# Kernel tuning notes

Hardware: AMD Instinct MI355X
Metric: run time of the kernel (lower is better)

## Reference

```python
import jax, jax.numpy as jnp
import numpy as np

N_HEAD, D_MODEL, D_K, D_V = 16, 1024, 64, 64
BIAS_WEIGHT = 1.0
NEG = -10000.0


def setup_inputs() -> dict:
    key = jax.random.key(0)
    ks = jax.random.split(key, 9)
    B, L = 2, 2048
    q = jax.random.normal(ks[0], (B, L, D_MODEL), dtype=jnp.float32)
    k = jax.random.normal(ks[1], (B, L, D_MODEL), dtype=jnp.float32)
    v = jax.random.normal(ks[2], (B, L, D_MODEL), dtype=jnp.float32)
    mask = jax.random.randint(ks[3], (B, L, L), 0, 2, dtype=jnp.int32)
    bias = jax.random.normal(ks[4], (B, L, L), dtype=jnp.float32)
    s = 1.0 / np.sqrt(D_MODEL)
    w_qs = jax.random.uniform(ks[5], (D_MODEL, N_HEAD * D_K), jnp.float32, -s, s)
    w_ks = jax.random.uniform(ks[6], (D_MODEL, N_HEAD * D_K), jnp.float32, -s, s)
    w_vs = jax.random.uniform(ks[7], (D_MODEL, N_HEAD * D_V), jnp.float32, -s, s)
    w_fc = jax.random.uniform(ks[8], (N_HEAD * D_V, D_MODEL), jnp.float32, -s, s)
    return {"q": q, "k": k, "v": v, "mask": mask, "bias": bias,
            "w_qs": w_qs, "w_ks": w_ks, "w_vs": w_vs, "w_fc": w_fc}


def reference(q, k, v, mask, bias, w_qs, w_ks, w_vs, w_fc):
    B, Lq, _ = q.shape
    # project and split heads: [B, H, L, d]
    qh = (q @ w_qs).reshape(B, Lq, N_HEAD, D_K).transpose(0, 2, 1, 3)
    kh = (k @ w_ks).reshape(B, k.shape[1], N_HEAD, D_K).transpose(0, 2, 1, 3)
    vh = (v @ w_vs).reshape(B, v.shape[1], N_HEAD, D_V).transpose(0, 2, 1, 3)
    temperature = D_K ** 0.5
    attn = jnp.einsum('bhqd,bhkd->bhqk', qh / temperature, kh)
    attn = attn + bias[:, None, :, :] * BIAS_WEIGHT
    attn = jnp.where(mask[:, None, :, :] == 0, NEG, attn)
    attn = jax.nn.softmax(attn, axis=-1)
    out = jnp.einsum('bhqk,bhkd->bhqd', attn, vh)
    out = out.transpose(0, 2, 1, 3).reshape(B, Lq, N_HEAD * D_V)
    return out @ w_fc
```

## Files before the change

kernel.cpp:

```cpp
#include <hip/hip_runtime.h>
#include <cstddef>

#define DEV static __device__ __forceinline__

typedef float f32x4 __attribute__((ext_vector_type(4)));
typedef __bf16 bf16x8 __attribute__((ext_vector_type(8)));
typedef __bf16 bf16x4v __attribute__((ext_vector_type(4)));
typedef unsigned short u16x8 __attribute__((ext_vector_type(8)));
typedef unsigned short u16x4 __attribute__((ext_vector_type(4)));
typedef unsigned u32x2 __attribute__((ext_vector_type(2)));
typedef unsigned u32x4 __attribute__((ext_vector_type(4)));
typedef _Float16 f16;
typedef _Float16 f16x4 __attribute__((ext_vector_type(4)));

constexpr int BB = 2, LL = 2048, DM = 1024, NH = 16, DK = 64;
constexpr float LOG2E = 1.44269504f;

DEV unsigned short f2bf(float f) {
  unsigned u = __builtin_bit_cast(unsigned, f);
  u += 0x7fffu + ((u >> 16) & 1u);
  return (unsigned short)(u >> 16);
}
DEV u16x4 cvt4(f32x4 v) {
  bf16x4v b = __builtin_convertvector(v, bf16x4v);
  return __builtin_bit_cast(u16x4, b);
}
DEV bf16x8 asbf(u16x8 v) { return __builtin_bit_cast(bf16x8, v); }
DEV f32x4 mfma16(u16x8 a, u16x8 b, f32x4 c) {
  return __builtin_amdgcn_mfma_f32_16x16x32_bf16(asbf(a), asbf(b), c, 0, 0, 0);
}
#if __has_builtin(__builtin_amdgcn_exp2f)
DEV float fexp2(float x) { return __builtin_amdgcn_exp2f(x); }
#else
DEV float fexp2(float x) { return exp2f(x); }
#endif
DEV void swap32(unsigned& a, unsigned& b) {
#if __has_builtin(__builtin_amdgcn_permlane32_swap)
  u32x2 r = __builtin_amdgcn_permlane32_swap(a, b, false, false);
  a = r[0]; b = r[1];
#else
  asm("v_permlane32_swap_b32 %0, %1" : "+v"(a), "+v"(b));
#endif
}
DEV void swap16(unsigned& a, unsigned& b) {
#if __has_builtin(__builtin_amdgcn_permlane16_swap)
  u32x2 r = __builtin_amdgcn_permlane16_swap(a, b, false, false);
  a = r[0]; b = r[1];
#else
  asm("v_permlane16_swap_b32 %0, %1" : "+v"(a), "+v"(b));
#endif
}
DEV void g2lds16(const void* g, void* l) {
  __builtin_amdgcn_global_load_lds(
      (const __attribute__((address_space(1))) unsigned int*)g,
      (__attribute__((address_space(3))) unsigned int*)l, 16, 0, 0);
}

__global__ __launch_bounds__(256) void prep_all(
    const float* __restrict__ w0, const float* __restrict__ w1,
    const float* __restrict__ w2, const float* __restrict__ w3,
    unsigned short* __restrict__ wT, const int* __restrict__ mask,
    const float* __restrict__ bias, f16* __restrict__ bmf,
    const float* __restrict__ s0, const float* __restrict__ s1,
    const float* __restrict__ s2, unsigned short* __restrict__ qkvb) {
  int f = blockIdx.x, t = threadIdx.x;
  if (f < 4096) {
    __shared__ float tile[32][33];
    int z = f >> 10, rem = f & 1023;
    int k0 = (rem >> 5) * 32, n0 = (rem & 31) * 32;
    const float* W = (z == 0) ? w0 : (z == 1) ? w1 : (z == 2) ? w2 : w3;
    unsigned short* out = wT + (size_t)z * DM * DM;
    int tx = t & 31, ty = t >> 5;
#pragma unroll
    for (int p = 0; p < 4; p++)
      tile[ty + 8 * p][tx] = W[(size_t)(k0 + ty + 8 * p) * DM + n0 + tx];
    __syncthreads();
#pragma unroll
    for (int p = 0; p < 4; p++)
      out[(size_t)(n0 + ty + 8 * p) * DM + k0 + tx] = f2bf(tile[tx][ty + 8 * p]);
  } else if (f < 12288) {
    int f2 = f - 4096;
    int w = t >> 6, lane = t & 63;
    int bq = f2 >> 5;
    int kt = (f2 & 31) * 4 + w;
    int b = bq >> 7, qt = bq & 127;
    int q = qt * 16 + (lane & 15);
    int k = kt * 16 + (lane >> 4) * 4;
    size_t src = ((size_t)b * LL + q) * LL + k;
    int4 mk = *(const int4*)(mask + src);
    float4 bs = *(const float4*)(bias + src);
    f16x4 o;
    o[0] = (f16)((mk.x == 0 ? -10000.f : bs.x) * LOG2E);
    o[1] = (f16)((mk.y == 0 ? -10000.f : bs.y) * LOG2E);
    o[2] = (f16)((mk.z == 0 ? -10000.f : bs.z) * LOG2E);
    o[3] = (f16)((mk.w == 0 ? -10000.f : bs.w) * LOG2E);
    *(f16x4*)(bmf + ((size_t)bq * 128 + kt) * 256 + lane * 4) = o;
  } else {
    int f3 = f - 12288;
    int z = f3 >> 11;
    const float* src = (z == 0) ? s0 : (z == 1) ? s1 : s2;
    size_t i = ((size_t)(f3 & 2047) * 256 + t) * 8;
    float4 a = *(const float4*)(src + i);
    float4 b = *(const float4*)(src + i + 4);
    u16x8 o;
    o[0] = f2bf(a.x); o[1] = f2bf(a.y); o[2] = f2bf(a.z); o[3] = f2bf(a.w);
    o[4] = f2bf(b.x); o[5] = f2bf(b.y); o[6] = f2bf(b.z); o[7] = f2bf(b.w);
    *(u16x8*)(qkvb + (size_t)z * (size_t)(BB * LL) * DM + i) = o;
  }
}

template <int KITERS>
DEV void gemm_core(const unsigned short* __restrict__ A,
                   const unsigned short* __restrict__ BT,
                   unsigned short* Al, unsigned short* Bl,
                   int m0, int n0, int k0beg, int t, f32x4 (&acc)[4][4]) {
  int lane = t & 63, c = lane & 15, qd = lane >> 4;
  int w = t >> 6, wm = w >> 1, wn = w & 1;
  int r0 = t >> 3;
  int gsw = (t & 7) ^ (r0 & 7);

#pragma unroll 1
  for (int kk = 0; kk < KITERS; ++kk) {
    int k0 = k0beg + kk * 64;
#pragma unroll
    for (int p = 0; p < 4; ++p) {
      g2lds16(&A[(size_t)(m0 + 32 * p + r0) * DM + k0 + 8 * gsw],
              &Al[p * 2048 + w * 512]);
      g2lds16(&BT[(size_t)(n0 + 32 * p + r0) * DM + k0 + 8 * gsw],
              &Bl[p * 2048 + w * 512]);
    }
    __syncthreads();
#pragma unroll
    for (int ks = 0; ks < 2; ++ks) {
      u16x8 af[4], bfr[4];
#pragma unroll
      for (int mt = 0; mt < 4; ++mt)
        af[mt] = *(const u16x8*)&Al[(64 * wm + 16 * mt + c) * 64 +
                                    (((4 * ks + qd) ^ (c & 7)) << 3)];
#pragma unroll
      for (int nt = 0; nt < 4; ++nt)
        bfr[nt] = *(const u16x8*)&Bl[(64 * wn + 16 * nt + c) * 64 +
                                     (((4 * ks + qd) ^ (c & 7)) << 3)];
#pragma unroll
      for (int mt = 0; mt < 4; ++mt)
#pragma unroll
        for (int nt = 0; nt < 4; ++nt)
          acc[mt][nt] = mfma16(af[mt], bfr[nt], acc[mt][nt]);
    }
    __syncthreads();
  }
}

__global__ __launch_bounds__(256, 3) void proj_gemm(
    const unsigned short* __restrict__ qkvb, const unsigned short* __restrict__ wT,
    unsigned short* __restrict__ qh, unsigned short* __restrict__ kh,
    unsigned short* __restrict__ vT) {
  __shared__ unsigned short Al[128 * 64];
  __shared__ unsigned short Bl[128 * 64];
  int o = blockIdx.x;
  int wg = (o & 7) * 96 + (o >> 3);
  int z = wg >> 8, rem = wg & 255;
  int m0 = (rem >> 3) * 128, n0 = (rem & 7) * 128;
  const unsigned short* A = qkvb + (size_t)z * BB * LL * DM;
  const unsigned short* BT = wT + (size_t)z * DM * DM;
  int t = threadIdx.x, lane = t & 63, c = lane & 15, qd = lane >> 4;
  int w = t >> 6, wm = w >> 1, wn = w & 1;
  f32x4 acc[4][4] = {};
  gemm_core<DM / 64>(A, BT, Al, Bl, m0, n0, 0, t, acc);

  if (z == 2) {
#pragma unroll
    for (int mt = 0; mt < 4; ++mt)
#pragma unroll
      for (int nt = 0; nt < 4; ++nt) {
        int n = n0 + 64 * wn + 16 * nt + c;
        int h = n >> 6, d = n & 63;
        int m = m0 + 64 * wm + 16 * mt + 4 * qd;
        int b = m >> 11, l = m & 2047;
        *(u16x4*)&vT[(((size_t)b * NH + h) * DK + d) * LL + l] = cvt4(acc[mt][nt]);
      }
  } else {
    unsigned short* Ch = z ? kh : qh;
    float scale = z ? 1.0f : 0.125f * LOG2E;
#pragma unroll
    for (int mt = 0; mt < 4; ++mt)
#pragma unroll
      for (int nt = 0; nt < 4; ++nt) {
        int n = n0 + 64 * wn + 16 * nt + c;
        int h = n >> 6, d = n & 63;
#pragma unroll
        for (int i = 0; i < 4; ++i) {
          int m = m0 + 64 * wm + 16 * mt + 4 * qd + i;
          int b = m >> 11, l = m & 2047;
          Ch[(((size_t)b * NH + h) * LL + l) * DK + d] = f2bf(acc[mt][nt][i] * scale);
        }
      }
  }
}

__global__ __launch_bounds__(256, 3) void fc_gemm(const unsigned short* __restrict__ A,
                                                  const unsigned short* __restrict__ BT,
                                                  float* __restrict__ C) {
  __shared__ unsigned short Al[128 * 64];
  __shared__ unsigned short Bl[128 * 64];
  int o = blockIdx.x;
  int wg = (o & 7) * 32 + (o >> 3);
  int m0 = (wg >> 3) * 128, n0 = (wg & 7) * 128;
  int t = threadIdx.x, lane = t & 63, c = lane & 15, qd = lane >> 4;
  int w = t >> 6, wm = w >> 1, wn = w & 1;
  f32x4 acc[4][4] = {};
  gemm_core<DM / 64>(A, BT, Al, Bl, m0, n0, 0, t, acc);
#pragma unroll
  for (int mt = 0; mt < 4; ++mt)
#pragma unroll
    for (int nt = 0; nt < 4; ++nt) {
      int n = n0 + 64 * wn + 16 * nt + c;
#pragma unroll
      for (int i = 0; i < 4; ++i) {
        int m = m0 + 64 * wm + 16 * mt + 4 * qd + i;
        C[(size_t)m * DM + n] = acc[mt][nt][i];
      }
    }
}

__global__ __launch_bounds__(256, 4) void attn_kern(
    const unsigned short* __restrict__ qh, const unsigned short* __restrict__ kh,
    const unsigned short* __restrict__ vT, const f16* __restrict__ bmf,
    unsigned short* __restrict__ O) {
  __shared__ unsigned short Kb[2][4096];
  __shared__ unsigned short Vb[3][4096];

  int t = threadIdx.x, w = t >> 6, lane = t & 63, c = lane & 15, qd = lane >> 4;
  int o = blockIdx.x;
  int wg = (o & 7) * 128 + (o >> 3);
  int x = wg & 31, h = (wg >> 5) & 15, b = wg >> 9;
  int q0 = x * 64;
  const unsigned short* Q = qh + (((size_t)b * NH + h) * LL + q0) * DK;
  const unsigned short* K = kh + ((size_t)b * NH + h) * LL * DK;
  const unsigned short* V = vT + ((size_t)b * NH + h) * DK * LL;
  const f16* BMF = bmf + (((size_t)b * 128 + x * 4 + w) * 128) * 256 + lane * 4;
  int rt = t >> 3, gg = t & 7;

  f16x4 bc[4], bn[4];
#pragma unroll
  for (int r = 0; r < 2; ++r) {
    int row = r * 32 + rt;
    int sc = ((gg ^ (row & 7)) << 3);
    g2lds16(&Q[(size_t)row * DK + sc], &Kb[1][r * 2048 + w * 512]);
    g2lds16(&K[(size_t)row * DK + sc], &Kb[0][r * 2048 + w * 512]);
    g2lds16(&V[(size_t)row * LL + sc], &Vb[0][r * 2048 + w * 512]);
  }
#pragma unroll
  for (int mt = 0; mt < 4; ++mt) bc[mt] = *(const f16x4*)&BMF[(size_t)mt * 256];
  __syncthreads();

  u16x8 qf[2];
#pragma unroll
  for (int ks = 0; ks < 2; ++ks)
    qf[ks] = *(const u16x8*)&Kb[1][(16 * w + c) * 64 +
                                   (((4 * ks + qd) ^ (c & 7)) << 3)];
  __syncthreads();

  {
#pragma unroll
    for (int r = 0; r < 2; ++r) {
      int row = r * 32 + rt;
      int sc = ((gg ^ (row & 7)) << 3);
      g2lds16(&K[(size_t)(64 + row) * DK + sc], &Kb[1][r * 2048 + w * 512]);
      g2lds16(&V[(size_t)row * LL + 64 + sc], &Vb[1][r * 2048 + w * 512]);
    }
#pragma unroll
    for (int mt = 0; mt < 4; ++mt)
      bn[mt] = *(const f16x4*)&BMF[(size_t)(4 + mt) * 256];
  }
  f32x4 sP[4];
  __builtin_amdgcn_s_setprio(1);
#pragma unroll
  for (int mt = 0; mt < 4; ++mt) {
    int row = 16 * mt + c;
    u16x8 k0f = *(const u16x8*)&Kb[0][row * 64 + ((qd ^ (c & 7)) << 3)];
    u16x8 k1f = *(const u16x8*)&Kb[0][row * 64 + (((4 + qd) ^ (c & 7)) << 3)];
    f16x4 b4 = bc[mt];
    f32x4 z = {(float)b4[0], (float)b4[1], (float)b4[2], (float)b4[3]};
    z = mfma16(k0f, qf[0], z);
    sP[mt] = mfma16(k1f, qf[1], z);
  }
  __builtin_amdgcn_s_setprio(0);
#pragma unroll
  for (int mt = 0; mt < 4; ++mt) bc[mt] = bn[mt];
  __syncthreads();

  const u16x8 ones = {0x3F80, 0x3F80, 0x3F80, 0x3F80,
                      0x3F80, 0x3F80, 0x3F80, 0x3F80};
  f32x4 lacc = {};
  f32x4 oacc[4] = {};
  unsigned short* Vr = Vb[0];
  unsigned short* Vc = Vb[1];
  unsigned short* Vw = Vb[2];

#pragma unroll 1
  for (int j = 1; j < 32; ++j) {
    const unsigned short* Kl = Kb[j & 1];
    unsigned short* Kw = Kb[(j + 1) & 1];
    if (j + 1 < 32) {
      int kt1 = (j + 1) * 64;
#pragma unroll
      for (int r = 0; r < 2; ++r) {
        int row = r * 32 + rt;
        int sc = ((gg ^ (row & 7)) << 3);
        g2lds16(&K[(size_t)(kt1 + row) * DK + sc], &Kw[r * 2048 + w * 512]);
        g2lds16(&V[(size_t)row * LL + kt1 + sc], &Vw[r * 2048 + w * 512]);
      }
#pragma unroll
      for (int mt = 0; mt < 4; ++mt)
        bn[mt] = *(const f16x4*)&BMF[(size_t)((j + 1) * 4 + mt) * 256];
    }

    __builtin_amdgcn_s_setprio(1);
    u16x8 pf[2];
    {
      unsigned L[4], H[4];
#pragma unroll
      for (int mt = 0; mt < 4; ++mt) {
        f32x4 p;
#pragma unroll
        for (int i = 0; i < 4; ++i) p[i] = fexp2(sP[mt][i]);
        u32x2 lw = __builtin_bit_cast(u32x2, cvt4(p));
        L[mt] = lw[0];
        H[mt] = lw[1];
      }
#pragma unroll
      for (int ks = 0; ks < 2; ++ks) {
        unsigned l0 = L[2 * ks], l1 = L[2 * ks + 1];
        unsigned h0 = H[2 * ks], h1 = H[2 * ks + 1];
        swap32(l0, l1); swap16(l0, l1);
        swap32(h0, h1); swap16(h0, h1);
        u32x4 pw = {l0, h0, l1, h1};
        pf[ks] = __builtin_bit_cast(u16x8, pw);
      }
    }
    f32x4 sN[4];
#pragma unroll
    for (int mt = 0; mt < 4; ++mt) {
      int row = 16 * mt + c;
      u16x8 k0f = *(const u16x8*)&Kl[row * 64 + ((qd ^ (c & 7)) << 3)];
      u16x8 k1f = *(const u16x8*)&Kl[row * 64 + (((4 + qd) ^ (c & 7)) << 3)];
      f16x4 b4 = bc[mt];
      f32x4 z = {(float)b4[0], (float)b4[1], (float)b4[2], (float)b4[3]};
      z = mfma16(k0f, qf[0], z);
      sN[mt] = mfma16(k1f, qf[1], z);
    }
    lacc = mfma16(ones, pf[0], lacc);
    lacc = mfma16(ones, pf[1], lacc);
#pragma unroll
    for (int dt = 0; dt < 4; ++dt) {
      int row = 16 * dt + c;
      u16x8 v0f = *(const u16x8*)&Vr[row * 64 + ((qd ^ (c & 7)) << 3)];
      u16x8 v1f = *(const u16x8*)&Vr[row * 64 + (((4 + qd) ^ (c & 7)) << 3)];
      oacc[dt] = mfma16(v0f, pf[0], oacc[dt]);
      oacc[dt] = mfma16(v1f, pf[1], oacc[dt]);
    }
    __builtin_amdgcn_s_setprio(0);

#pragma unroll
    for (int mt = 0; mt < 4; ++mt) { sP[mt] = sN[mt]; bc[mt] = bn[mt]; }
    unsigned short* tv = Vr; Vr = Vc; Vc = Vw; Vw = tv;
    __syncthreads();
  }

  {
    u16x8 pf[2];
    unsigned L[4], H[4];
#pragma unroll
    for (int mt = 0; mt < 4; ++mt) {
      f32x4 p;
#pragma unroll
      for (int i = 0; i < 4; ++i) p[i] = fexp2(sP[mt][i]);
      u32x2 lw = __builtin_bit_cast(u32x2, cvt4(p));
      L[mt] = lw[0]; H[mt] = lw[1];
    }
#pragma unroll
    for (int ks = 0; ks < 2; ++ks) {
      unsigned l0 = L[2 * ks], l1 = L[2 * ks + 1];
      unsigned h0 = H[2 * ks], h1 = H[2 * ks + 1];
      swap32(l0, l1); swap16(l0, l1);
      swap32(h0, h1); swap16(h0, h1);
      u32x4 pw = {l0, h0, l1, h1};
      pf[ks] = __builtin_bit_cast(u16x8, pw);
    }
    lacc = mfma16(ones, pf[0], lacc);
    lacc = mfma16(ones, pf[1], lacc);
#pragma unroll
    for (int dt = 0; dt < 4; ++dt) {
      int row = 16 * dt + c;
      u16x8 v0f = *(const u16x8*)&Vr[row * 64 + ((qd ^ (c & 7)) << 3)];
      u16x8 v1f = *(const u16x8*)&Vr[row * 64 + (((4 + qd) ^ (c & 7)) << 3)];
      oacc[dt] = mfma16(v0f, pf[0], oacc[dt]);
      oacc[dt] = mfma16(v1f, pf[1], oacc[dt]);
    }
  }

  {
    float rl = 1.f / lacc[0];
    size_t orow = ((size_t)b * LL + q0 + 16 * w + c) * DM + h * DK;
#pragma unroll
    for (int dt = 0; dt < 4; ++dt)
      *(u16x4*)&O[orow + 16 * dt + 4 * qd] = cvt4(oacc[dt] * rl);
  }
}

extern "C" void kernel_launch(void* const* d_in, const int* in_sizes, int n_in,
                              void* d_out, int out_size, void* d_ws, size_t ws_size,
                              hipStream_t stream) {
  (void)in_sizes; (void)n_in; (void)ws_size; (void)out_size;
  const float* q = (const float*)d_in[0];
  const float* k = (const float*)d_in[1];
  const float* v = (const float*)d_in[2];
  const int* mask = (const int*)d_in[3];
  const float* bias = (const float*)d_in[4];
  const float* w_qs = (const float*)d_in[5];
  const float* w_ks = (const float*)d_in[6];
  const float* w_vs = (const float*)d_in[7];
  const float* w_fc = (const float*)d_in[8];

  char* ws = (char*)d_ws;
  const size_t MB = 1024 * 1024;
  unsigned short* wT = (unsigned short*)(ws);
  f16* bmf = (f16*)(ws + 8 * MB);
  unsigned short* qkvb = (unsigned short*)(ws + 24 * MB);
  unsigned short* qh = (unsigned short*)(ws + 48 * MB);
  unsigned short* kh = (unsigned short*)(ws + 56 * MB);
  unsigned short* vhT = (unsigned short*)(ws + 64 * MB);
  unsigned short* Obuf = (unsigned short*)(ws + 72 * MB);

  prep_all<<<dim3(18432), dim3(256), 0, stream>>>(w_qs, w_ks, w_vs, w_fc, wT,
                                                  mask, bias, bmf, q, k, v, qkvb);
  proj_gemm<<<dim3(768), 256, 0, stream>>>(qkvb, wT, qh, kh, vhT);
  attn_kern<<<dim3(1024), dim3(256), 0, stream>>>(qh, kh, vhT, bmf, Obuf);
  fc_gemm<<<dim3(256), 256, 0, stream>>>(Obuf, wT + (size_t)3 * DM * DM,
                                         (float*)d_out);
}
```

Before: 267.1 us.

## Overlap mask/bias prep with projection GEMM and halve fc_gemm tile M

Moves the mask+bias to fp16 conversion out of prep_all and appends it as extra blocks (index 768 and up) in the proj_gemm launch. Those bandwidth-bound blocks can then run alongside the compute-bound GEMM tiles. Separately, fc_gemm switches to 64x128 tiles with 512 blocks, so the 256-block launch no longer underfills the CUs. The trade-off is more B-tile reloads in fc_gemm and mixed block types within one kernel, which may affect scheduling and LDS occupancy.

Result: faster. 256.2 us (-4.1%).

```diff
diff --git a/kernel.cpp b/kernel.cpp
--- a/kernel.cpp
+++ b/kernel.cpp
@@ -59,10 +59,9 @@
 __global__ __launch_bounds__(256) void prep_all(
     const float* __restrict__ w0, const float* __restrict__ w1,
     const float* __restrict__ w2, const float* __restrict__ w3,
-    unsigned short* __restrict__ wT, const int* __restrict__ mask,
-    const float* __restrict__ bias, f16* __restrict__ bmf,
-    const float* __restrict__ s0, const float* __restrict__ s1,
-    const float* __restrict__ s2, unsigned short* __restrict__ qkvb) {
+    unsigned short* __restrict__ wT, const float* __restrict__ s0,
+    const float* __restrict__ s1, const float* __restrict__ s2,
+    unsigned short* __restrict__ qkvb) {
   int f = blockIdx.x, t = threadIdx.x;
   if (f < 4096) {
     __shared__ float tile[32][33];
@@ -78,8 +77,72 @@
 #pragma unroll
     for (int p = 0; p < 4; p++)
       out[(size_t)(n0 + ty + 8 * p) * DM + k0 + tx] = f2bf(tile[tx][ty + 8 * p]);
-  } else if (f < 12288) {
-    int f2 = f - 4096;
+  } else {
+    int f3 = f - 4096;
+    int z = f3 >> 11;
+    const float* src = (z == 0) ? s0 : (z == 1) ? s1 : s2;
+    size_t i = ((size_t)(f3 & 2047) * 256 + t) * 8;
+    float4 a = *(const float4*)(src + i);
+    float4 b = *(const float4*)(src + i + 4);
+    u16x8 o;
+    o[0] = f2bf(a.x); o[1] = f2bf(a.y); o[2] = f2bf(a.z); o[3] = f2bf(a.w);
+    o[4] = f2bf(b.x); o[5] = f2bf(b.y); o[6] = f2bf(b.z); o[7] = f2bf(b.w);
+    *(u16x8*)(qkvb + (size_t)z * (size_t)(BB * LL) * DM + i) = o;
+  }
+}
+
+template <int KITERS>
+DEV void gemm_core(const unsigned short* __restrict__ A,
+                   const unsigned short* __restrict__ BT,
+                   unsigned short* Al, unsigned short* Bl,
+                   int m0, int n0, int k0beg, int t, f32x4 (&acc)[4][4]) {
+  int lane = t & 63, c = lane & 15, qd = lane >> 4;
+  int w = t >> 6, wm = w >> 1, wn = w & 1;
+  int r0 = t >> 3;
+  int gsw = (t & 7) ^ (r0 & 7);
+
+#pragma unroll 1
+  for (int kk = 0; kk < KITERS; ++kk) {
+    int k0 = k0beg + kk * 64;
+#pragma unroll
+    for (int p = 0; p < 4; ++p) {
+      g2lds16(&A[(size_t)(m0 + 32 * p + r0) * DM + k0 + 8 * gsw],
+              &Al[p * 2048 + w * 512]);
+      g2lds16(&BT[(size_t)(n0 + 32 * p + r0) * DM + k0 + 8 * gsw],
+              &Bl[p * 2048 + w * 512]);
+    }
+    __syncthreads();
+#pragma unroll
+    for (int ks = 0; ks < 2; ++ks) {
+      u16x8 af[4], bfr[4];
+#pragma unroll
+      for (int mt = 0; mt < 4; ++mt)
+        af[mt] = *(const u16x8*)&Al[(64 * wm + 16 * mt + c) * 64 +
+                                    (((4 * ks + qd) ^ (c & 7)) << 3)];
+#pragma unroll
+      for (int nt = 0; nt < 4; ++nt)
+        bfr[nt] = *(const u16x8*)&Bl[(64 * wn + 16 * nt + c) * 64 +
+                                     (((4 * ks + qd) ^ (c & 7)) << 3)];
+#pragma unroll
+      for (int mt = 0; mt < 4; ++mt)
+#pragma unroll
+        for (int nt = 0; nt < 4; ++nt)
+          acc[mt][nt] = mfma16(af[mt], bfr[nt], acc[mt][nt]);
+    }
+    __syncthreads();
+  }
+}
+
+__global__ __launch_bounds__(256, 3) void proj_gemm(
+    const unsigned short* __restrict__ qkvb, const unsigned short* __restrict__ wT,
+    unsigned short* __restrict__ qh, unsigned short* __restrict__ kh,
+    unsigned short* __restrict__ vT, const int* __restrict__ mask,
+    const float* __restrict__ bias, f16* __restrict__ bmf) {
+  __shared__ unsigned short Al[128 * 64];
+  __shared__ unsigned short Bl[128 * 64];
+  int o = blockIdx.x, t = threadIdx.x;
+  if (o >= 768) {
+    int f2 = o - 768;
     int w = t >> 6, lane = t & 63;
     int bq = f2 >> 5;
     int kt = (f2 & 31) * 4 + w;
@@ -89,81 +152,20 @@
     size_t src = ((size_t)b * LL + q) * LL + k;
     int4 mk = *(const int4*)(mask + src);
     float4 bs = *(const float4*)(bias + src);
-    f16x4 o;
-    o[0] = (f16)((mk.x == 0 ? -10000.f : bs.x) * LOG2E);
-    o[1] = (f16)((mk.y == 0 ? -10000.f : bs.y) * LOG2E);
-    o[2] = (f16)((mk.z == 0 ? -10000.f : bs.z) * LOG2E);
-    o[3] = (f16)((mk.w == 0 ? -10000.f : bs.w) * LOG2E);
-    *(f16x4*)(bmf + ((size_t)bq * 128 + kt) * 256 + lane * 4) = o;
-  } else {
-    int f3 = f - 12288;
-    int z = f3 >> 11;
-    const float* src = (z == 0) ? s0 : (z == 1) ? s1 : s2;
-    size_t i = ((size_t)(f3 & 2047) * 256 + t) * 8;
-    float4 a = *(const float4*)(src + i);
-    float4 b = *(const float4*)(src + i + 4);
-    u16x8 o;
-    o[0] = f2bf(a.x); o[1] = f2bf(a.y); o[2] = f2bf(a.z); o[3] = f2bf(a.w);
-    o[4] = f2bf(b.x); o[5] = f2bf(b.y); o[6] = f2bf(b.z); o[7] = f2bf(b.w);
-    *(u16x8*)(qkvb + (size_t)z * (size_t)(BB * LL) * DM + i) = o;
-  }
-}
-
-template <int KITERS>
-DEV void gemm_core(const unsigned short* __restrict__ A,
-                   const unsigned short* __restrict__ BT,
-                   unsigned short* Al, unsigned short* Bl,
-                   int m0, int n0, int k0beg, int t, f32x4 (&acc)[4][4]) {
-  int lane = t & 63, c = lane & 15, qd = lane >> 4;
-  int w = t >> 6, wm = w >> 1, wn = w & 1;
-  int r0 = t >> 3;
-  int gsw = (t & 7) ^ (r0 & 7);
-
-#pragma unroll 1
-  for (int kk = 0; kk < KITERS; ++kk) {
-    int k0 = k0beg + kk * 64;
-#pragma unroll
-    for (int p = 0; p < 4; ++p) {
-      g2lds16(&A[(size_t)(m0 + 32 * p + r0) * DM + k0 + 8 * gsw],
-              &Al[p * 2048 + w * 512]);
-      g2lds16(&BT[(size_t)(n0 + 32 * p + r0) * DM + k0 + 8 * gsw],
-              &Bl[p * 2048 + w * 512]);
-    }
-    __syncthreads();
-#pragma unroll
-    for (int ks = 0; ks < 2; ++ks) {
-      u16x8 af[4], bfr[4];
-#pragma unroll
-      for (int mt = 0; mt < 4; ++mt)
-        af[mt] = *(const u16x8*)&Al[(64 * wm + 16 * mt + c) * 64 +
-                                    (((4 * ks + qd) ^ (c & 7)) << 3)];
-#pragma unroll
-      for (int nt = 0; nt < 4; ++nt)
-        bfr[nt] = *(const u16x8*)&Bl[(64 * wn + 16 * nt + c) * 64 +
-                                     (((4 * ks + qd) ^ (c & 7)) << 3)];
-#pragma unroll
-      for (int mt = 0; mt < 4; ++mt)
-#pragma unroll
-        for (int nt = 0; nt < 4; ++nt)
-          acc[mt][nt] = mfma16(af[mt], bfr[nt], acc[mt][nt]);
-    }
-    __syncthreads();
-  }
-}
-
-__global__ __launch_bounds__(256, 3) void proj_gemm(
-    const unsigned short* __restrict__ qkvb, const unsigned short* __restrict__ wT,
-    unsigned short* __restrict__ qh, unsigned short* __restrict__ kh,
-    unsigned short* __restrict__ vT) {
-  __shared__ unsigned short Al[128 * 64];
-  __shared__ unsigned short Bl[128 * 64];
-  int o = blockIdx.x;
+    f16x4 oo;
+    oo[0] = (f16)((mk.x == 0 ? -10000.f : bs.x) * LOG2E);
+    oo[1] = (f16)((mk.y == 0 ? -10000.f : bs.y) * LOG2E);
+    oo[2] = (f16)((mk.z == 0 ? -10000.f : bs.z) * LOG2E);
+    oo[3] = (f16)((mk.w == 0 ? -10000.f : bs.w) * LOG2E);
+    *(f16x4*)(bmf + ((size_t)bq * 128 + kt) * 256 + lane * 4) = oo;
+    return;
+  }
   int wg = (o & 7) * 96 + (o >> 3);
   int z = wg >> 8, rem = wg & 255;
   int m0 = (rem >> 3) * 128, n0 = (rem & 7) * 128;
   const unsigned short* A = qkvb + (size_t)z * BB * LL * DM;
   const unsigned short* BT = wT + (size_t)z * DM * DM;
-  int t = threadIdx.x, lane = t & 63, c = lane & 15, qd = lane >> 4;
+  int lane = t & 63, c = lane & 15, qd = lane >> 4;
   int w = t >> 6, wm = w >> 1, wn = w & 1;
   f32x4 acc[4][4] = {};
   gemm_core<DM / 64>(A, BT, Al, Bl, m0, n0, 0, t, acc);
@@ -198,26 +200,59 @@
   }
 }
 
-__global__ __launch_bounds__(256, 3) void fc_gemm(const unsigned short* __restrict__ A,
+__global__ __launch_bounds__(256, 2) void fc_gemm(const unsigned short* __restrict__ A,
                                                   const unsigned short* __restrict__ BT,
                                                   float* __restrict__ C) {
-  __shared__ unsigned short Al[128 * 64];
+  __shared__ unsigned short Al[64 * 64];
   __shared__ unsigned short Bl[128 * 64];
   int o = blockIdx.x;
-  int wg = (o & 7) * 32 + (o >> 3);
-  int m0 = (wg >> 3) * 128, n0 = (wg & 7) * 128;
+  int wg = (o & 7) * 64 + (o >> 3);
+  int m0 = (wg >> 3) * 64, n0 = (wg & 7) * 128;
   int t = threadIdx.x, lane = t & 63, c = lane & 15, qd = lane >> 4;
   int w = t >> 6, wm = w >> 1, wn = w & 1;
-  f32x4 acc[4][4] = {};
-  gemm_core<DM / 64>(A, BT, Al, Bl, m0, n0, 0, t, acc);
-#pragma unroll
-  for (int mt = 0; mt < 4; ++mt)
+  int r0 = t >> 3, gsw = (t & 7) ^ (r0 & 7);
+  f32x4 acc[2][4] = {};
+
+#pragma unroll 1
+  for (int kk = 0; kk < 16; ++kk) {
+    int k0 = kk * 64;
+#pragma unroll
+    for (int p = 0; p < 2; ++p)
+      g2lds16(&A[(size_t)(m0 + 32 * p + r0) * DM + k0 + 8 * gsw],
+              &Al[p * 2048 + w * 512]);
+#pragma unroll
+    for (int p = 0; p < 4; ++p)
+      g2lds16(&BT[(size_t)(n0 + 32 * p + r0) * DM + k0 + 8 * gsw],
+              &Bl[p * 2048 + w * 512]);
+    __syncthreads();
+#pragma unroll
+    for (int ks = 0; ks < 2; ++ks) {
+      u16x8 af[2], bfr[4];
+#pragma unroll
+      for (int mt = 0; mt < 2; ++mt)
+        af[mt] = *(const u16x8*)&Al[(32 * wm + 16 * mt + c) * 64 +
+                                    (((4 * ks + qd) ^ (c & 7)) << 3)];
+#pragma unroll
+      for (int nt = 0; nt < 4; ++nt)
+        bfr[nt] = *(const u16x8*)&Bl[(64 * wn + 16 * nt + c) * 64 +
+                                     (((4 * ks + qd) ^ (c & 7)) << 3)];
+#pragma unroll
+      for (int mt = 0; mt < 2; ++mt)
+#pragma unroll
+        for (int nt = 0; nt < 4; ++nt)
+          acc[mt][nt] = mfma16(af[mt], bfr[nt], acc[mt][nt]);
+    }
+    __syncthreads();
+  }
+
+#pragma unroll
+  for (int mt = 0; mt < 2; ++mt)
 #pragma unroll
     for (int nt = 0; nt < 4; ++nt) {
       int n = n0 + 64 * wn + 16 * nt + c;
 #pragma unroll
       for (int i = 0; i < 4; ++i) {
-        int m = m0 + 64 * wm + 16 * mt + 4 * qd + i;
+        int m = m0 + 32 * wm + 16 * mt + 4 * qd + i;
         C[(size_t)m * DM + n] = acc[mt][nt][i];
       }
     }
@@ -433,10 +468,11 @@
   unsigned short* vhT = (unsigned short*)(ws + 64 * MB);
   unsigned short* Obuf = (unsigned short*)(ws + 72 * MB);
 
-  prep_all<<<dim3(18432), dim3(256), 0, stream>>>(w_qs, w_ks, w_vs, w_fc, wT,
-                                                  mask, bias, bmf, q, k, v, qkvb);
-  proj_gemm<<<dim3(768), 256, 0, stream>>>(qkvb, wT, qh, kh, vhT);
+  prep_all<<<dim3(10240), dim3(256), 0, stream>>>(w_qs, w_ks, w_vs, w_fc, wT,
+                                                  q, k, v, qkvb);
+  proj_gemm<<<dim3(8960), 256, 0, stream>>>(qkvb, wT, qh, kh, vhT, mask, bias,
+                                            bmf);
   attn_kern<<<dim3(1024), dim3(256), 0, stream>>>(qh, kh, vhT, bmf, Obuf);
-  fc_gemm<<<dim3(256), 256, 0, stream>>>(Obuf, wT + (size_t)3 * DM * DM,
+  fc_gemm<<<dim3(512), 256, 0, stream>>>(Obuf, wT + (size_t)3 * DM * DM,
                                          (float*)d_out);
 }
```
